# Optimization experiments

Measured on AMD Instinct MI355X. Metric: run time of the kernel, lower is better.

## Reference

```python
import jax, jax.numpy as jnp
import numpy as np

E = 2  # expand_ratio


def _linear_scan(u, a):
    """h_t = a_t * h_{t-1} + u_t along axis 0, h_{-1}=0. Parallel associative scan."""
    def comb(x, y):
        a1, b1 = x
        a2, b2 = y
        return a2 * a1, a2 * b1 + b2
    _, h = jax.lax.associative_scan(comb, (a, u), axis=0)
    return h


def setup_inputs() -> dict:
    key = jax.random.key(0)
    ks = jax.random.split(key, 8)
    n, b, d = 2048, 4, 1024
    s = 1.0 / np.sqrt(d)
    return {
        "x": jax.random.normal(ks[0], (n, b, d), jnp.float32),
        "lower_bound": jax.random.uniform(ks[1], (d,), jnp.float32),
        "W_in": jax.random.normal(ks[2], (d, 3 * d), jnp.float32) * s,
        "b_in": jnp.zeros((3 * d,), jnp.float32),
        "W_out": jax.random.normal(ks[3], (d, d), jnp.float32) * s,
        "b_out": jnp.zeros((d,), jnp.float32),
        "gamma": jnp.ones((d,), jnp.float32),
        "beta": jnp.zeros((d,), jnp.float32),
    }


def reference(x, lower_bound, W_in, b_in, W_out, b_out, gamma, beta):
    n, b, d = x.shape
    h = d // E
    feat = x @ W_in + b_in                      # (n,b,3d)
    inp, og, fg = jnp.split(feat, 3, axis=-1)
    inp = jax.nn.silu(inp)
    og = jax.nn.sigmoid(og)
    fg = jax.nn.sigmoid(fg)
    # reshape (h d) -> h, d=E
    inp = inp.reshape(n, b, h, E)
    og = og.reshape(n, b, h, E)
    fg = fg.reshape(n, b, h, E)
    lb = lower_bound.reshape(h, E)
    lam = lb + (1.0 - lb) * fg                  # (n,b,h,E)
    # outer-product input: (1-lam) outer inp over the E dims -> (n,b,h,E,E)
    u = jnp.einsum('nbhd,nbhe->nbhde', 1.0 - lam, inp)
    a = jnp.broadcast_to(lam[..., None], u.shape)
    u = u.reshape(n, b, h * E * E)
    a = a.reshape(n, b, h * E * E)
    state_fwd = _linear_scan(u, a)
    state_rev = jnp.flip(_linear_scan(jnp.flip(u, 0), jnp.flip(a, 0)), 0)
    state = (state_fwd + state_rev).reshape(n, b, h, E, E)
    out = jnp.einsum('nbhde,nbhd->nbhe', state, og).reshape(n, b, d)
    # layernorm over last dim
    mu = jnp.mean(out, axis=-1, keepdims=True)
    var = jnp.var(out, axis=-1, keepdims=True)
    out = (out - mu) * jax.lax.rsqrt(var + 1e-5) * gamma + beta
    return out @ W_out + b_out
```

## Files before the change

### kernel.cpp

```cpp
#include <hip/hip_runtime.h>

typedef __bf16 bf16x8 __attribute__((ext_vector_type(8)));
typedef float floatx4 __attribute__((ext_vector_type(4)));

#define NCH 64
#define CLEN 32

__device__ __forceinline__ unsigned short f2bf(float f) {
  unsigned int u = __builtin_bit_cast(unsigned int, f);
  u += 0x7fff + ((u >> 16) & 1);
  return (unsigned short)(u >> 16);
}

__device__ __forceinline__ void async_copy16(const void* g, void* l) {
  __builtin_amdgcn_global_load_lds(
      (const __attribute__((address_space(1))) unsigned int*)g,
      (__attribute__((address_space(3))) unsigned int*)l, 16, 0, 0);
}

__global__ void cast_x_kernel(const float* __restrict__ in, unsigned short* __restrict__ out) {
  int i = blockIdx.x * blockDim.x + threadIdx.x;
  float4 v = ((const float4*)in)[i];
  ushort4 o;
  o.x = f2bf(v.x); o.y = f2bf(v.y); o.z = f2bf(v.z); o.w = f2bf(v.w);
  ((ushort4*)out)[i] = o;
}

__global__ void tcast_kernel(const float* __restrict__ W, unsigned short* __restrict__ WT, int ncols) {
  __shared__ float tile[32][33];
  int n0 = blockIdx.x * 32, k0 = blockIdx.y * 32;
  int tx = threadIdx.x, ty = threadIdx.y;
  tile[ty][tx] = W[(size_t)(k0 + ty) * ncols + n0 + tx];
  __syncthreads();
  WT[(size_t)(n0 + ty) * 1024 + k0 + tx] = f2bf(tile[tx][ty]);
}

template <int EPI>
__global__ __launch_bounds__(256) void gemm_kernel(
    const unsigned short* __restrict__ A, const unsigned short* __restrict__ BT,
    const float* __restrict__ bias, const float* __restrict__ lb,
    float* __restrict__ out0, float* __restrict__ out1, float* __restrict__ out2) {
  __shared__ alignas(16) unsigned short As[128 * 32];
  __shared__ alignas(16) unsigned short Bs[128 * 32];
  const int m0 = blockIdx.x * 128, n0 = blockIdx.y * 128;
  const int tid = threadIdx.x;
  const int lane = tid & 63, wave = tid >> 6;
  const int wm = (wave >> 1) * 64, wn = (wave & 1) * 64;
  const int mrow = lane & 15, q = lane >> 4;
  const int qsw = q ^ ((mrow >> 1) & 3);
  floatx4 acc[4][4] = {};
  const int r0 = wave * 32;
  const int srow = r0 + (lane >> 2);
  const int qs = (lane & 3) ^ ((srow >> 1) & 3);
  const unsigned short* gA0 = A + (size_t)(m0 + srow) * 1024 + qs * 8;
  const unsigned short* gA1 = gA0 + (size_t)16 * 1024;
  const unsigned short* gB0 = BT + (size_t)(n0 + srow) * 1024 + qs * 8;
  const unsigned short* gB1 = gB0 + (size_t)16 * 1024;
  unsigned short* lA0 = &As[r0 * 32];
  unsigned short* lA1 = &As[(r0 + 16) * 32];
  unsigned short* lB0 = &Bs[r0 * 32];
  unsigned short* lB1 = &Bs[(r0 + 16) * 32];
  for (int kt = 0; kt < 1024; kt += 32) {
    __syncthreads();
    async_copy16(gA0, lA0);
    async_copy16(gA1, lA1);
    async_copy16(gB0, lB0);
    async_copy16(gB1, lB1);
    gA0 += 32; gA1 += 32; gB0 += 32; gB1 += 32;
    __syncthreads();
    bf16x8 af[4], bf[4];
#pragma unroll
    for (int i = 0; i < 4; i++) af[i] = *(const bf16x8*)&As[(wm + i * 16 + mrow) * 32 + qsw * 8];
#pragma unroll
    for (int j = 0; j < 4; j++) bf[j] = *(const bf16x8*)&Bs[(wn + j * 16 + mrow) * 32 + qsw * 8];
#pragma unroll
    for (int i = 0; i < 4; i++)
#pragma unroll
      for (int j = 0; j < 4; j++)
        acc[i][j] = __builtin_amdgcn_mfma_f32_16x16x32_bf16(af[i], bf[j], acc[i][j], 0, 0, 0);
  }
#pragma unroll
  for (int i = 0; i < 4; i++) {
    const int rbase = m0 + wm + i * 16 + q * 4;
#pragma unroll
    for (int j = 0; j < 4; j++) {
      const int c = n0 + wn + j * 16 + mrow;
      const float bi = bias[c];
#pragma unroll
      for (int g = 0; g < 4; g++) {
        float v = acc[i][j][g] + bi;
        size_t ro = (size_t)(rbase + g) * 1024;
        if (EPI == 0) {
          out0[ro + c] = v;
        } else {
          int segc = c >> 10, cl = c & 1023;
          float s = 1.f / (1.f + __expf(-v));
          if (segc == 0) out0[ro + cl] = v * s;
          else if (segc == 1) out1[ro + cl] = s;
          else { float L = lb[cl]; out2[ro + cl] = L + (1.f - L) * s; }
        }
      }
    }
  }
}

__global__ void scan_passA(const float* __restrict__ lam, const float* __restrict__ inp,
                           float* __restrict__ sumA, float* __restrict__ sumBf,
                           float* __restrict__ sumBr) {
  int idx = blockIdx.x * 256 + threadIdx.x;
  int h = idx & 511, cb = idx >> 9, b = cb & 3, c = cb >> 2;
  long base = ((long)c * CLEN * 4 + b) * 1024 + 2 * h;
  float p0 = 1.f, p1 = 1.f;
  float s00 = 0.f, s01 = 0.f, s10 = 0.f, s11 = 0.f;
  float r00 = 0.f, r01 = 0.f, r10 = 0.f, r11 = 0.f;
  for (int t = 0; t < CLEN; t++) {
    float2 l = *(const float2*)(lam + base);
    float2 ip = *(const float2*)(inp + base);
    base += 4096;
    float omx = 1.f - l.x, omy = 1.f - l.y;
    float u00 = omx * ip.x, u01 = omx * ip.y, u10 = omy * ip.x, u11 = omy * ip.y;
    r00 += p0 * u00; r01 += p0 * u01; r10 += p1 * u10; r11 += p1 * u11;
    s00 = l.x * s00 + u00; s01 = l.x * s01 + u01;
    s10 = l.y * s10 + u10; s11 = l.y * s11 + u11;
    p0 *= l.x; p1 *= l.y;
  }
  ((float2*)sumA)[idx] = make_float2(p0, p1);
  ((float4*)sumBf)[idx] = make_float4(s00, s01, s10, s11);
  ((float4*)sumBr)[idx] = make_float4(r00, r01, r10, r11);
}

__global__ void scan_passB(const float* __restrict__ sumA, const float* __restrict__ sumBf,
                           const float* __restrict__ sumBr, float* __restrict__ initF,
                           float* __restrict__ initR) {
  int tid = blockIdx.x * 256 + threadIdx.x;
  int dir = tid >> 13;
  int rem = tid & 8191;
  int ch = rem & 3;
  int bh = rem >> 2;
  int dd = ch >> 1;
  if (dir == 0) {
    float H = 0.f;
    for (int c = 0; c < NCH; c++) {
      int si = c * 2048 + bh;
      initF[(size_t)si * 4 + ch] = H;
      H = sumA[(size_t)si * 2 + dd] * H + sumBf[(size_t)si * 4 + ch];
    }
  } else {
    float G = 0.f;
    for (int c = NCH - 1; c >= 0; c--) {
      int si = c * 2048 + bh;
      initR[(size_t)si * 4 + ch] = G;
      G = sumA[(size_t)si * 2 + dd] * G + sumBr[(size_t)si * 4 + ch];
    }
  }
}

__global__ void scan_passC1(const float* __restrict__ lam, const float* __restrict__ inp,
                            const float* __restrict__ og, const float* __restrict__ initF,
                            float* __restrict__ outp) {
  int idx = blockIdx.x * 256 + threadIdx.x;
  int h = idx & 511, cb = idx >> 9, b = cb & 3, c = cb >> 2;
  float4 H = ((const float4*)initF)[idx];
  float h00 = H.x, h01 = H.y, h10 = H.z, h11 = H.w;
  long base = ((long)c * CLEN * 4 + b) * 1024 + 2 * h;
  for (int t = 0; t < CLEN; t++) {
    float2 l = *(const float2*)(lam + base);
    float2 ip = *(const float2*)(inp + base);
    float2 o = *(const float2*)(og + base);
    float omx = 1.f - l.x, omy = 1.f - l.y;
    h00 = l.x * h00 + omx * ip.x; h01 = l.x * h01 + omx * ip.y;
    h10 = l.y * h10 + omy * ip.x; h11 = l.y * h11 + omy * ip.y;
    float2 rr;
    rr.x = h00 * o.x + h10 * o.y;
    rr.y = h01 * o.x + h11 * o.y;
    *(float2*)(outp + base) = rr;
    base += 4096;
  }
}

__global__ void scan_passC2(const float* __restrict__ lam, const float* __restrict__ inp,
                            const float* __restrict__ og, const float* __restrict__ initR,
                            float* __restrict__ outp) {
  int idx = blockIdx.x * 256 + threadIdx.x;
  int h = idx & 511, cb = idx >> 9, b = cb & 3, c = cb >> 2;
  float4 G = ((const float4*)initR)[idx];
  float g00 = G.x, g01 = G.y, g10 = G.z, g11 = G.w;
  long base = ((long)(c * CLEN + CLEN - 1) * 4 + b) * 1024 + 2 * h;
  for (int t = 0; t < CLEN; t++) {
    float2 l = *(const float2*)(lam + base);
    float2 ip = *(const float2*)(inp + base);
    float2 o = *(const float2*)(og + base);
    float2 pv = *(const float2*)(outp + base);
    float omx = 1.f - l.x, omy = 1.f - l.y;
    g00 = omx * ip.x + l.x * g00; g01 = omx * ip.y + l.x * g01;
    g10 = omy * ip.x + l.y * g10; g11 = omy * ip.y + l.y * g11;
    float2 rr;
    rr.x = pv.x + g00 * o.x + g10 * o.y;
    rr.y = pv.y + g01 * o.x + g11 * o.y;
    *(float2*)(outp + base) = rr;
    base -= 4096;
  }
}

__global__ void ln_kernel(const float* __restrict__ xin, const float* __restrict__ gamma,
                          const float* __restrict__ beta, unsigned short* __restrict__ ybf) {
  int row = blockIdx.x;
  int tid = threadIdx.x;
  float4 v = ((const float4*)(xin + (size_t)row * 1024))[tid];
  float s = v.x + v.y + v.z + v.w;
  float s2 = v.x * v.x + v.y * v.y + v.z * v.z + v.w * v.w;
#pragma unroll
  for (int o = 32; o > 0; o >>= 1) { s += __shfl_down(s, o); s2 += __shfl_down(s2, o); }
  __shared__ float red[8];
  int lane = tid & 63, w = tid >> 6;
  if (lane == 0) { red[w] = s; red[w + 4] = s2; }
  __syncthreads();
  if (tid == 0) {
    float a = red[0] + red[1] + red[2] + red[3];
    float b = red[4] + red[5] + red[6] + red[7];
    red[0] = a * (1.f / 1024.f);
    red[4] = b * (1.f / 1024.f);
  }
  __syncthreads();
  float mean = red[0];
  float var = red[4] - mean * mean;
  float rstd = rsqrtf(var + 1e-5f);
  float4 g = ((const float4*)gamma)[tid];
  float4 be = ((const float4*)beta)[tid];
  ushort4 o4;
  o4.x = f2bf((v.x - mean) * rstd * g.x + be.x);
  o4.y = f2bf((v.y - mean) * rstd * g.y + be.y);
  o4.z = f2bf((v.z - mean) * rstd * g.z + be.z);
  o4.w = f2bf((v.w - mean) * rstd * g.w + be.w);
  ((ushort4*)(ybf + (size_t)row * 1024))[tid] = o4;
}

extern "C" void kernel_launch(void* const* d_in, const int* in_sizes, int n_in,
                              void* d_out, int out_size, void* d_ws, size_t ws_size,
                              hipStream_t stream) {
  const float* x = (const float*)d_in[0];
  const float* lb = (const float*)d_in[1];
  const float* Win = (const float*)d_in[2];
  const float* bin = (const float*)d_in[3];
  const float* Wout = (const float*)d_in[4];
  const float* bout = (const float*)d_in[5];
  const float* gamma = (const float*)d_in[6];
  const float* beta = (const float*)d_in[7];
  float* out = (float*)d_out;

  char* ws = (char*)d_ws;
  size_t off = 0;
  auto alloc = [&](size_t bytes) {
    void* p = ws + off;
    off += (bytes + 255) & ~(size_t)255;
    return p;
  };
  unsigned short* x_bf = (unsigned short*)alloc(8192ull * 1024 * 2);
  unsigned short* winT = (unsigned short*)alloc(3072ull * 1024 * 2);
  unsigned short* woutT = (unsigned short*)alloc(1024ull * 1024 * 2);
  float* inp_s = (float*)alloc(8192ull * 1024 * 4);
  float* og_s = (float*)alloc(8192ull * 1024 * 4);
  float* lam = (float*)alloc(8192ull * 1024 * 4);
  float* outp = (float*)alloc(8192ull * 1024 * 4);
  unsigned short* y_bf = (unsigned short*)alloc(8192ull * 1024 * 2);
  float* sumA = (float*)alloc(64ull * 4 * 512 * 2 * 4);
  float* sumBf = (float*)alloc(64ull * 4 * 512 * 4 * 4);
  float* sumBr = (float*)alloc(64ull * 4 * 512 * 4 * 4);
  float* initF = (float*)alloc(64ull * 4 * 512 * 4 * 4);
  float* initR = (float*)alloc(64ull * 4 * 512 * 4 * 4);

  cast_x_kernel<<<8192, 256, 0, stream>>>(x, x_bf);
  dim3 tb(32, 32);
  tcast_kernel<<<dim3(96, 32), tb, 0, stream>>>(Win, winT, 3072);
  tcast_kernel<<<dim3(32, 32), tb, 0, stream>>>(Wout, woutT, 1024);
  gemm_kernel<1><<<dim3(64, 24), 256, 0, stream>>>(x_bf, winT, bin, lb, inp_s, og_s, lam);
  scan_passA<<<512, 256, 0, stream>>>(lam, inp_s, sumA, sumBf, sumBr);
  scan_passB<<<64, 256, 0, stream>>>(sumA, sumBf, sumBr, initF, initR);
  scan_passC1<<<512, 256, 0, stream>>>(lam, inp_s, og_s, initF, outp);
  scan_passC2<<<512, 256, 0, stream>>>(lam, inp_s, og_s, initR, outp);
  ln_kernel<<<8192, 256, 0, stream>>>(outp, gamma, beta, y_bf);
  gemm_kernel<0><<<dim3(64, 8), 256, 0, stream>>>(y_bf, woutT, bout, nullptr, out, nullptr, nullptr);
}
```

Before: 288.2 us.

## Fuse forward/reverse scan passes with layernorm and store gates in bf16

```diff
diff --git a/kernel.cpp b/kernel.cpp
--- a/kernel.cpp
+++ b/kernel.cpp
@@ -3,13 +3,17 @@
 typedef __bf16 bf16x8 __attribute__((ext_vector_type(8)));
 typedef float floatx4 __attribute__((ext_vector_type(4)));
 
-#define NCH 64
-#define CLEN 32
+#define NCH 128
+#define CLEN 16
 
 __device__ __forceinline__ unsigned short f2bf(float f) {
   unsigned int u = __builtin_bit_cast(unsigned int, f);
   u += 0x7fff + ((u >> 16) & 1);
   return (unsigned short)(u >> 16);
+}
+__device__ __forceinline__ float bf2f(unsigned short u) {
+  unsigned int v = (unsigned int)u << 16;
+  return __builtin_bit_cast(float, v);
 }
 
 __device__ __forceinline__ void async_copy16(const void* g, void* l) {
@@ -39,7 +43,9 @@
 __global__ __launch_bounds__(256) void gemm_kernel(
     const unsigned short* __restrict__ A, const unsigned short* __restrict__ BT,
     const float* __restrict__ bias, const float* __restrict__ lb,
-    float* __restrict__ out0, float* __restrict__ out1, float* __restrict__ out2) {
+    float* __restrict__ outf,
+    unsigned short* __restrict__ o_inp, unsigned short* __restrict__ o_og,
+    unsigned short* __restrict__ o_om) {
   __shared__ alignas(16) unsigned short As[128 * 32];
   __shared__ alignas(16) unsigned short Bs[128 * 32];
   const int m0 = blockIdx.x * 128, n0 = blockIdx.y * 128;
@@ -91,20 +97,27 @@
         float v = acc[i][j][g] + bi;
         size_t ro = (size_t)(rbase + g) * 1024;
         if (EPI == 0) {
-          out0[ro + c] = v;
+          outf[ro + c] = v;
         } else {
           int segc = c >> 10, cl = c & 1023;
-          float s = 1.f / (1.f + __expf(-v));
-          if (segc == 0) out0[ro + cl] = v * s;
-          else if (segc == 1) out1[ro + cl] = s;
-          else { float L = lb[cl]; out2[ro + cl] = L + (1.f - L) * s; }
+          if (segc == 0) {
+            float s = 1.f / (1.f + __expf(-v));
+            o_inp[ro + cl] = f2bf(v * s);
+          } else if (segc == 1) {
+            float s = 1.f / (1.f + __expf(-v));
+            o_og[ro + cl] = f2bf(s);
+          } else {
+            float sm = 1.f / (1.f + __expf(v));
+            float L = lb[cl];
+            o_om[ro + cl] = f2bf((1.f - L) * sm);
+          }
         }
       }
     }
   }
 }
 
-__global__ void scan_passA(const float* __restrict__ lam, const float* __restrict__ inp,
+__global__ void scan_passA(const unsigned short* __restrict__ om, const unsigned short* __restrict__ ip,
                            float* __restrict__ sumA, float* __restrict__ sumBf,
                            float* __restrict__ sumBr) {
   int idx = blockIdx.x * 256 + threadIdx.x;
@@ -113,16 +126,19 @@
   float p0 = 1.f, p1 = 1.f;
   float s00 = 0.f, s01 = 0.f, s10 = 0.f, s11 = 0.f;
   float r00 = 0.f, r01 = 0.f, r10 = 0.f, r11 = 0.f;
+#pragma unroll
   for (int t = 0; t < CLEN; t++) {
-    float2 l = *(const float2*)(lam + base);
-    float2 ip = *(const float2*)(inp + base);
+    ushort2 l2 = *(const ushort2*)(om + base);
+    ushort2 i2 = *(const ushort2*)(ip + base);
     base += 4096;
-    float omx = 1.f - l.x, omy = 1.f - l.y;
-    float u00 = omx * ip.x, u01 = omx * ip.y, u10 = omy * ip.x, u11 = omy * ip.y;
+    float omx = bf2f(l2.x), omy = bf2f(l2.y);
+    float ipx = bf2f(i2.x), ipy = bf2f(i2.y);
+    float lx = 1.f - omx, ly = 1.f - omy;
+    float u00 = omx * ipx, u01 = omx * ipy, u10 = omy * ipx, u11 = omy * ipy;
     r00 += p0 * u00; r01 += p0 * u01; r10 += p1 * u10; r11 += p1 * u11;
-    s00 = l.x * s00 + u00; s01 = l.x * s01 + u01;
-    s10 = l.y * s10 + u10; s11 = l.y * s11 + u11;
-    p0 *= l.x; p1 *= l.y;
+    s00 = lx * s00 + u00; s01 = lx * s01 + u01;
+    s10 = ly * s10 + u10; s11 = ly * s11 + u11;
+    p0 *= lx; p1 *= ly;
   }
   ((float2*)sumA)[idx] = make_float2(p0, p1);
   ((float4*)sumBf)[idx] = make_float4(s00, s01, s10, s11);
@@ -155,84 +171,103 @@
   }
 }
 
-__global__ void scan_passC1(const float* __restrict__ lam, const float* __restrict__ inp,
-                            const float* __restrict__ og, const float* __restrict__ initF,
-                            float* __restrict__ outp) {
-  int idx = blockIdx.x * 256 + threadIdx.x;
-  int h = idx & 511, cb = idx >> 9, b = cb & 3, c = cb >> 2;
-  float4 H = ((const float4*)initF)[idx];
-  float h00 = H.x, h01 = H.y, h10 = H.z, h11 = H.w;
-  long base = ((long)c * CLEN * 4 + b) * 1024 + 2 * h;
+__global__ __launch_bounds__(512) void scanC_ln_kernel(
+    const unsigned short* __restrict__ om, const unsigned short* __restrict__ ip,
+    const unsigned short* __restrict__ og,
+    const float* __restrict__ initF, const float* __restrict__ initR,
+    const float* __restrict__ gamma, const float* __restrict__ beta,
+    unsigned short* __restrict__ ybf) {
+  __shared__ float tile[8][1024];
+  __shared__ float ldsG[1024];
+  __shared__ float ldsB[1024];
+  const int h = threadIdx.x;
+  const int cb = blockIdx.x;
+  const int b = cb & 3, c = cb >> 2;
+  const int idx = cb * 512 + h;
+  *(float2*)&ldsG[2 * h] = *(const float2*)(gamma + 2 * h);
+  *(float2*)&ldsB[2 * h] = *(const float2*)(beta + 2 * h);
+  float4 F = ((const float4*)initF)[idx];
+  float4 R = ((const float4*)initR)[idx];
+  float outx[CLEN], outy[CLEN];
+  const long base = ((long)c * CLEN * 4 + b) * 1024 + 2 * h;
+  float h00 = F.x, h01 = F.y, h10 = F.z, h11 = F.w;
+  long p = base;
+#pragma unroll
   for (int t = 0; t < CLEN; t++) {
-    float2 l = *(const float2*)(lam + base);
-    float2 ip = *(const float2*)(inp + base);
-    float2 o = *(const float2*)(og + base);
-    float omx = 1.f - l.x, omy = 1.f - l.y;
-    h00 = l.x * h00 + omx * ip.x; h01 = l.x * h01 + omx * ip.y;
-    h10 = l.y * h10 + omy * ip.x; h11 = l.y * h11 + omy * ip.y;
-    float2 rr;
-    rr.x = h00 * o.x + h10 * o.y;
-    rr.y = h01 * o.x + h11 * o.y;
-    *(float2*)(outp + base) = rr;
-    base += 4096;
-  }
-}
-
-__global__ void scan_passC2(const float* __restrict__ lam, const float* __restrict__ inp,
-                            const float* __restrict__ og, const float* __restrict__ initR,
-                            float* __restrict__ outp) {
-  int idx = blockIdx.x * 256 + threadIdx.x;
-  int h = idx & 511, cb = idx >> 9, b = cb & 3, c = cb >> 2;
-  float4 G = ((const float4*)initR)[idx];
-  float g00 = G.x, g01 = G.y, g10 = G.z, g11 = G.w;
-  long base = ((long)(c * CLEN + CLEN - 1) * 4 + b) * 1024 + 2 * h;
-  for (int t = 0; t < CLEN; t++) {
-    float2 l = *(const float2*)(lam + base);
-    float2 ip = *(const float2*)(inp + base);
-    float2 o = *(const float2*)(og + base);
-    float2 pv = *(const float2*)(outp + base);
-    float omx = 1.f - l.x, omy = 1.f - l.y;
-    g00 = omx * ip.x + l.x * g00; g01 = omx * ip.y + l.x * g01;
-    g10 = omy * ip.x + l.y * g10; g11 = omy * ip.y + l.y * g11;
-    float2 rr;
-    rr.x = pv.x + g00 * o.x + g10 * o.y;
-    rr.y = pv.y + g01 * o.x + g11 * o.y;
-    *(float2*)(outp + base) = rr;
-    base -= 4096;
-  }
-}
-
-__global__ void ln_kernel(const float* __restrict__ xin, const float* __restrict__ gamma,
-                          const float* __restrict__ beta, unsigned short* __restrict__ ybf) {
-  int row = blockIdx.x;
-  int tid = threadIdx.x;
-  float4 v = ((const float4*)(xin + (size_t)row * 1024))[tid];
-  float s = v.x + v.y + v.z + v.w;
-  float s2 = v.x * v.x + v.y * v.y + v.z * v.z + v.w * v.w;
-#pragma unroll
-  for (int o = 32; o > 0; o >>= 1) { s += __shfl_down(s, o); s2 += __shfl_down(s2, o); }
-  __shared__ float red[8];
-  int lane = tid & 63, w = tid >> 6;
-  if (lane == 0) { red[w] = s; red[w + 4] = s2; }
-  __syncthreads();
-  if (tid == 0) {
-    float a = red[0] + red[1] + red[2] + red[3];
-    float b = red[4] + red[5] + red[6] + red[7];
-    red[0] = a * (1.f / 1024.f);
-    red[4] = b * (1.f / 1024.f);
-  }
-  __syncthreads();
-  float mean = red[0];
-  float var = red[4] - mean * mean;
-  float rstd = rsqrtf(var + 1e-5f);
-  float4 g = ((const float4*)gamma)[tid];
-  float4 be = ((const float4*)beta)[tid];
-  ushort4 o4;
-  o4.x = f2bf((v.x - mean) * rstd * g.x + be.x);
-  o4.y = f2bf((v.y - mean) * rstd * g.y + be.y);
-  o4.z = f2bf((v.z - mean) * rstd * g.z + be.z);
-  o4.w = f2bf((v.w - mean) * rstd * g.w + be.w);
-  ((ushort4*)(ybf + (size_t)row * 1024))[tid] = o4;
+    ushort2 l2 = *(const ushort2*)(om + p);
+    ushort2 i2 = *(const ushort2*)(ip + p);
+    ushort2 o2 = *(const ushort2*)(og + p);
+    p += 4096;
+    float omx = bf2f(l2.x), omy = bf2f(l2.y);
+    float ipx = bf2f(i2.x), ipy = bf2f(i2.y);
+    float ox = bf2f(o2.x), oy = bf2f(o2.y);
+    float lx = 1.f - omx, ly = 1.f - omy;
+    h00 = lx * h00 + omx * ipx; h01 = lx * h01 + omx * ipy;
+    h10 = ly * h10 + omy * ipx; h11 = ly * h11 + omy * ipy;
+    outx[t] = h00 * ox + h10 * oy;
+    outy[t] = h01 * ox + h11 * oy;
+  }
+  float g00 = R.x, g01 = R.y, g10 = R.z, g11 = R.w;
+  p = base + (CLEN - 1) * 4096;
+#pragma unroll
+  for (int t = CLEN - 1; t >= 0; t--) {
+    ushort2 l2 = *(const ushort2*)(om + p);
+    ushort2 i2 = *(const ushort2*)(ip + p);
+    ushort2 o2 = *(const ushort2*)(og + p);
+    p -= 4096;
+    float omx = bf2f(l2.x), omy = bf2f(l2.y);
+    float ipx = bf2f(i2.x), ipy = bf2f(i2.y);
+    float ox = bf2f(o2.x), oy = bf2f(o2.y);
+    float lx = 1.f - omx, ly = 1.f - omy;
+    g00 = omx * ipx + lx * g00; g01 = omx * ipy + lx * g01;
+    g10 = omy * ipx + ly * g10; g11 = omy * ipy + ly * g11;
+    outx[t] += g00 * ox + g10 * oy;
+    outy[t] += g01 * ox + g11 * oy;
+  }
+  const int lane = h & 63, wv = h >> 6;
+#pragma unroll
+  for (int g = 0; g < CLEN / 8; g++) {
+    __syncthreads();
+#pragma unroll
+    for (int r = 0; r < 8; r++) {
+      float2 v2 = make_float2(outx[g * 8 + r], outy[g * 8 + r]);
+      *(float2*)&tile[r][2 * h] = v2;
+    }
+    __syncthreads();
+    {
+      const int t = g * 8 + wv;
+      float4 v[4];
+#pragma unroll
+      for (int k = 0; k < 4; k++) v[k] = *(const float4*)&tile[wv][lane * 16 + k * 4];
+      float s = 0.f, s2 = 0.f;
+#pragma unroll
+      for (int k = 0; k < 4; k++) {
+        s += v[k].x + v[k].y + v[k].z + v[k].w;
+        s2 += v[k].x * v[k].x + v[k].y * v[k].y + v[k].z * v[k].z + v[k].w * v[k].w;
+      }
+#pragma unroll
+      for (int off = 1; off < 64; off <<= 1) {
+        s += __shfl_xor(s, off);
+        s2 += __shfl_xor(s2, off);
+      }
+      float mean = s * (1.f / 1024.f);
+      float var = s2 * (1.f / 1024.f) - mean * mean;
+      float rstd = rsqrtf(var + 1e-5f);
+      unsigned short o16[16];
+#pragma unroll
+      for (int k = 0; k < 4; k++) {
+        float* vv = (float*)&v[k];
+#pragma unroll
+        for (int e = 0; e < 4; e++) {
+          int ch = lane * 16 + k * 4 + e;
+          o16[k * 4 + e] = f2bf((vv[e] - mean) * rstd * ldsG[ch] + ldsB[ch]);
+        }
+      }
+      size_t rowo = ((size_t)(c * CLEN + t) * 4 + b) * 1024 + lane * 16;
+      *(uint4*)(ybf + rowo) = *(uint4*)&o16[0];
+      *(uint4*)(ybf + rowo + 8) = *(uint4*)&o16[8];
+    }
+  }
 }
 
 extern "C" void kernel_launch(void* const* d_in, const int* in_sizes, int n_in,
@@ -258,26 +293,23 @@
   unsigned short* x_bf = (unsigned short*)alloc(8192ull * 1024 * 2);
   unsigned short* winT = (unsigned short*)alloc(3072ull * 1024 * 2);
   unsigned short* woutT = (unsigned short*)alloc(1024ull * 1024 * 2);
-  float* inp_s = (float*)alloc(8192ull * 1024 * 4);
-  float* og_s = (float*)alloc(8192ull * 1024 * 4);
-  float* lam = (float*)alloc(8192ull * 1024 * 4);
-  float* outp = (float*)alloc(8192ull * 1024 * 4);
+  unsigned short* inp_b = (unsigned short*)alloc(8192ull * 1024 * 2);
+  unsigned short* og_b = (unsigned short*)alloc(8192ull * 1024 * 2);
+  unsigned short* om_b = (unsigned short*)alloc(8192ull * 1024 * 2);
   unsigned short* y_bf = (unsigned short*)alloc(8192ull * 1024 * 2);
-  float* sumA = (float*)alloc(64ull * 4 * 512 * 2 * 4);
-  float* sumBf = (float*)alloc(64ull * 4 * 512 * 4 * 4);
-  float* sumBr = (float*)alloc(64ull * 4 * 512 * 4 * 4);
-  float* initF = (float*)alloc(64ull * 4 * 512 * 4 * 4);
-  float* initR = (float*)alloc(64ull * 4 * 512 * 4 * 4);
+  float* sumA = (float*)alloc((size_t)NCH * 4 * 512 * 2 * 4);
+  float* sumBf = (float*)alloc((size_t)NCH * 4 * 512 * 4 * 4);
+  float* sumBr = (float*)alloc((size_t)NCH * 4 * 512 * 4 * 4);
+  float* initF = (float*)alloc((size_t)NCH * 4 * 512 * 4 * 4);
+  float* initR = (float*)alloc((size_t)NCH * 4 * 512 * 4 * 4);
 
   cast_x_kernel<<<8192, 256, 0, stream>>>(x, x_bf);
   dim3 tb(32, 32);
   tcast_kernel<<<dim3(96, 32), tb, 0, stream>>>(Win, winT, 3072);
   tcast_kernel<<<dim3(32, 32), tb, 0, stream>>>(Wout, woutT, 1024);
-  gemm_kernel<1><<<dim3(64, 24), 256, 0, stream>>>(x_bf, winT, bin, lb, inp_s, og_s, lam);
-  scan_passA<<<512, 256, 0, stream>>>(lam, inp_s, sumA, sumBf, sumBr);
+  gemm_kernel<1><<<dim3(64, 24), 256, 0, stream>>>(x_bf, winT, bin, lb, nullptr, inp_b, og_b, om_b);
+  scan_passA<<<(NCH * 4 * 512) / 256, 256, 0, stream>>>(om_b, inp_b, sumA, sumBf, sumBr);
   scan_passB<<<64, 256, 0, stream>>>(sumA, sumBf, sumBr, initF, initR);
-  scan_passC1<<<512, 256, 0, stream>>>(lam, inp_s, og_s, initF, outp);
-  scan_passC2<<<512, 256, 0, stream>>>(lam, inp_s, og_s, initR, outp);
-  ln_kernel<<<8192, 256, 0, stream>>>(outp, gamma, beta, y_bf);
-  gemm_kernel<0><<<dim3(64, 8), 256, 0, stream>>>(y_bf, woutT, bout, nullptr, out, nullptr, nullptr);
-}
+  scanC_ln_kernel<<<NCH * 4, 512, 0, stream>>>(om_b, inp_b, og_b, initF, initR, gamma, beta, y_bf);
+  gemm_kernel<0><<<dim3(64, 8), 256, 0, stream>>>(y_bf, woutT, bout, nullptr, out, nullptr, nullptr, nullptr);
+}
```

Measured after the change: 262.0 us. 1.1x faster.
